# Optimization experiments

Hardware: AMD Instinct MI355X
Metric: run time of the kernel (lower is better)

The kernel has to match this reference:

```python
import jax, jax.numpy as jnp
import numpy as np
from jax import lax

K = 3        # kernel_size
PAD = 1      # padding
DIL = 1      # dilation
C_IN = 64
C_OUT = 64
B, H, W = 8, 128, 128


def conv2d(x, w, b, pad):
    # x: [n,c,h,w], w: [o,i,kh,kw], pad: (ph, pw)
    out = lax.conv_general_dilated(
        x, w, window_strides=(1, 1),
        padding=[(pad[0], pad[0]), (pad[1], pad[1])],
        rhs_dilation=(DIL, DIL),
        dimension_numbers=("NCHW", "OIHW", "NCHW"))
    return out + b[None, :, None, None]


def bilinear_sample(x, py, px):
    # x: [n,c,h,w]; py/px: [n,K,h,w] fractional sample coords (zeros outside).
    n, c, h, w = x.shape
    y0 = jnp.floor(py)
    x0 = jnp.floor(px)
    wy = py - y0  # frac weights
    wx = px - x0
    xf = x.reshape(n, c, h * w)

    def gather(yi, xi):
        valid = ((yi >= 0) & (yi < h) & (xi >= 0) & (xi < w)).astype(x.dtype)
        yc = jnp.clip(yi, 0, h - 1).astype(jnp.int32)
        xc = jnp.clip(xi, 0, w - 1).astype(jnp.int32)
        idx = (yc * w + xc).reshape(n, -1)  # [n, K*h*w]
        g = jax.vmap(lambda xb, ib: jnp.take(xb, ib, axis=1))(xf, idx)
        return g.reshape(n, c, *yi.shape[1:]), valid

    v00, m00 = gather(y0, x0)
    v01, m01 = gather(y0, x0 + 1)
    v10, m10 = gather(y0 + 1, x0)
    v11, m11 = gather(y0 + 1, x0 + 1)
    w00 = ((1 - wy) * (1 - wx) * m00)[:, None]
    w01 = ((1 - wy) * wx * m01)[:, None]
    w10 = (wy * (1 - wx) * m10)[:, None]
    w11 = (wy * wx * m11)[:, None]
    return v00 * w00 + v01 * w01 + v10 * w10 + v11 * w11  # [n,c,K,h,w]


def deform_conv_axial(x, offset, mask, w, b, ky_base, kx_base):
    # offset: [n,K,2,h,w] (dy, dx per tap); mask: [n,K,h,w]
    # ky_base/kx_base: [K] static tap displacements
    n, c, h, wd = x.shape
    ii = jnp.arange(h, dtype=x.dtype)[None, None, :, None]
    jj = jnp.arange(wd, dtype=x.dtype)[None, None, None, :]
    py = ii + ky_base[None, :, None, None] + offset[:, :, 0]
    px = jj + kx_base[None, :, None, None] + offset[:, :, 1]
    val = bilinear_sample(x, py, px) * mask[:, None]  # [n,c,K,h,w]
    out = jnp.einsum('nckhw,ock->nohw', val, w.reshape(w.shape[0], c, K))
    return out + b[None, :, None, None]


def setup_inputs() -> dict:
    key = jax.random.key(0)
    ks = jax.random.split(key, 14)
    sc = 0.05
    d = {
        'x': jax.random.normal(ks[0], (B, C_IN, H, W), dtype=jnp.float32),
        'w_off_h': jax.random.normal(ks[1], (2 * K, C_IN, 1, K), dtype=jnp.float32) * sc,
        'b_off_h': jnp.zeros((2 * K,), dtype=jnp.float32),
        'w_mask_h': jax.random.normal(ks[2], (K, C_IN, 1, K), dtype=jnp.float32) * sc,
        'b_mask_h': jnp.zeros((K,), dtype=jnp.float32),
        'w_off_v': jax.random.normal(ks[3], (2 * K, C_IN, K, 1), dtype=jnp.float32) * sc,
        'b_off_v': jnp.zeros((2 * K,), dtype=jnp.float32),
        'w_mask_v': jax.random.normal(ks[4], (K, C_IN, K, 1), dtype=jnp.float32) * sc,
        'b_mask_v': jnp.zeros((K,), dtype=jnp.float32),
        'w_h': jax.random.normal(ks[5], (C_OUT, C_IN, 1, K), dtype=jnp.float32) * (1.0 / np.sqrt(C_IN * K)),
        'b_h': jax.random.normal(ks[6], (C_OUT,), dtype=jnp.float32) * 0.01,
        'w_v': jax.random.normal(ks[7], (C_OUT, C_OUT, K, 1), dtype=jnp.float32) * (1.0 / np.sqrt(C_OUT * K)),
        'b_v': jax.random.normal(ks[8], (C_OUT,), dtype=jnp.float32) * 0.01,
    }
    return d


def reference(x, w_off_h, b_off_h, w_mask_h, b_mask_h, w_off_v, b_off_v,
              w_mask_v, b_mask_v, w_h, b_h, w_v, b_v):
    n, c, h, w = x.shape
    taps = jnp.arange(K, dtype=x.dtype) * DIL - PAD  # [-1,0,1] for K=3,pad=1
    zeros_k = jnp.zeros((K,), dtype=x.dtype)

    # Horizontal pass: offsets/masks from x, deformable (1,K) conv on x
    offset_h = conv2d(x, w_off_h, b_off_h, (0, PAD)).reshape(n, K, 2, h, w)
    mask_h = jax.nn.sigmoid(conv2d(x, w_mask_h, b_mask_h, (0, PAD)))  # [n,K,h,w]
    x_h = deform_conv_axial(x, offset_h, mask_h, w_h, b_h, zeros_k, taps)

    # Vertical pass: offsets/masks from x, deformable (K,1) conv on x_h
    offset_v = conv2d(x, w_off_v, b_off_v, (PAD, 0)).reshape(n, K, 2, h, w)
    mask_v = jax.nn.sigmoid(conv2d(x, w_mask_v, b_mask_v, (PAD, 0)))
    x_v = deform_conv_axial(x_h, offset_v, mask_v, w_v, b_v, taps, zeros_k)
    return x_v
```

## Files before the change

kernel.cpp:

```cpp
#include <hip/hip_runtime.h>

#define C_ 64
#define H_ 128
#define W_ 128
#define B_ 8
#define HW_ (H_*W_)
#define NPIX (B_*HW_)

typedef _Float16 half8 __attribute__((ext_vector_type(8)));
typedef _Float16 half4 __attribute__((ext_vector_type(4)));
typedef float floatx4 __attribute__((ext_vector_type(4)));

#define RDL_I(v, l) __builtin_amdgcn_readlane((v), (l))
#define RDL_F(v, l) __builtin_bit_cast(float, \
    __builtin_amdgcn_readlane(__builtin_bit_cast(int, (v)), (l)))

__global__ __launch_bounds__(256, 8) void setup_kernel(
    const float* __restrict__ x, _Float16* __restrict__ xT,
    const float* __restrict__ w_off_h, const float* __restrict__ w_mask_h,
    const float* __restrict__ w_off_v, const float* __restrict__ w_mask_v,
    const float* __restrict__ w_h, const float* __restrict__ w_v,
    float* __restrict__ wOffAll, _Float16* __restrict__ wF16_h,
    _Float16* __restrict__ wF16_v)
{
    int gid = blockIdx.x * 256 + threadIdx.x;
    if (gid < 64 * 56) {
        int c = gid / 56, idx = gid - 56 * c;
        float v = 0.f;
        if (idx < 18)      v = w_off_h [((idx      ) / 3) * 192 + c * 3 + (idx      ) % 3];
        else if (idx < 27) v = w_mask_h[((idx - 18) / 3) * 192 + c * 3 + (idx - 18) % 3];
        else if (idx < 45) v = w_off_v [((idx - 27) / 3) * 192 + c * 3 + (idx - 27) % 3];
        else if (idx < 54) v = w_mask_v[((idx - 45) / 3) * 192 + c * 3 + (idx - 45) % 3];
        wOffAll[c * 56 + idx] = v;
    } else if (gid < 3584 + 24576) {
        int i = gid - 3584;
        if (i < 12288) {
            int o = i / 192, rem = i - o * 192;
            int c = rem / 3, k = rem - 3 * c;
            wF16_h[o * 192 + k * 64 + c] = (_Float16)w_h[i];
        } else {
            i -= 12288;
            int o = i / 192, rem = i - o * 192;
            int c = rem / 3, k = rem - 3 * c;
            wF16_v[o * 192 + k * 64 + c] = (_Float16)w_v[i];
        }
    }

    __shared__ _Float16 tile[64][66];
    int lane = threadIdx.x & 63;
    int wv   = threadIdx.x >> 6;
    int bid = blockIdx.x;
    int n = bid & 7;
    int m = bid >> 3;
    const float* xs = x + (size_t)n * C_ * HW_ + (size_t)m * 64;
    #pragma unroll
    for (int cc = 0; cc < 16; ++cc) {
        int c = wv * 16 + cc;
        tile[c][lane] = (_Float16)xs[(size_t)c * HW_ + lane];
    }
    __syncthreads();
    _Float16* xd = xT + ((size_t)n * HW_ + (size_t)m * 64) * 64;
    #pragma unroll
    for (int pp = 0; pp < 16; ++pp) {
        int p = wv * 16 + pp;
        xd[(size_t)p * 64 + lane] = tile[lane][p];
    }
}

#define SWIZZLE_NP()                        \
    int bid = blockIdx.x;                   \
    int n   = bid & 7;                      \
    int m   = bid >> 3;       \
    int pix = m * 64 + lane;                \
    int j = pix & (W_ - 1);                 \
    int i = pix >> 7;

#define TAP_WAVE48(DYE, DXE, MME, KYO, KXO)                                   \
    int   tI  = 0;                                                            \
    float tw0 = 0.f, tw1 = 0.f, tw2 = 0.f, tw3 = 0.f;                         \
    {                                                                         \
        int li = lane / 3, k = lane - 3 * li;                                 \
        if (lane < 48) {                                                      \
            int p = (li < 8) ? (wv * 8 + li) : (32 + wv * 8 + (li - 8));      \
            int pixp = m * 64 + p;                                            \
            float dy = (DYE);                                                 \
            float dx = (DXE);                                                 \
            float mm = (MME);                                                 \
            float fi = (float)(pixp >> 7), fj = (float)(pixp & (W_ - 1));     \
            float py = fi + (float)(KYO) + dy;                                \
            float px = fj + (float)(KXO) + dx;                                \
            float y0f = floorf(py), x0f = floorf(px);                         \
            float wy = py - y0f, wx = px - x0f;                               \
            int y0 = (int)y0f, x0 = (int)x0f;                                 \
            int y1 = y0 + 1, x1 = x0 + 1;                                     \
            bool vy0 = (y0 >= 0) && (y0 < H_);                                \
            bool vy1 = (y1 >= 0) && (y1 < H_);                                \
            bool vx0 = (x0 >= 0) && (x0 < W_);                                \
            bool vx1 = (x1 >= 0) && (x1 < W_);                                \
            float wy1 = 1.f - wy, wx1 = 1.f - wx;                             \
            float w00 = (vy0 && vx0) ? wy1 * wx1 * mm : 0.f;                  \
            float w01 = (vy0 && vx1) ? wy1 * wx  * mm : 0.f;                  \
            float w10 = (vy1 && vx0) ? wy  * wx1 * mm : 0.f;                  \
            float w11 = (vy1 && vx1) ? wy  * wx  * mm : 0.f;                  \
            int y0c = min(max(y0, 0), H_ - 1), y1c = min(max(y1, 0), H_ - 1); \
            int x0c = min(max(x0, 0), W_ - 1), x1c = min(max(x1, 0), W_ - 1); \
            int yb = min(max(y0, 0), H_ - 2),  xb = min(max(x0, 0), W_ - 2);  \
            int r0 = y0c - yb, r1 = y1c - yb;                   \
            int cA = x0c - xb, cB = x1c - xb;                   \
            tw0 = ((r0==0)&&(cA==0)?w00:0.f) + ((r0==0)&&(cB==0)?w01:0.f)     \
                + ((r1==0)&&(cA==0)?w10:0.f) + ((r1==0)&&(cB==0)?w11:0.f);    \
            tw1 = ((r0==0)&&(cA==1)?w00:0.f) + ((r0==0)&&(cB==1)?w01:0.f)     \
                + ((r1==0)&&(cA==1)?w10:0.f) + ((r1==0)&&(cB==1)?w11:0.f);    \
            tw2 = ((r0==1)&&(cA==0)?w00:0.f) + ((r0==1)&&(cB==0)?w01:0.f)     \
                + ((r1==1)&&(cA==0)?w10:0.f) + ((r1==1)&&(cB==0)?w11:0.f);    \
            tw3 = ((r0==1)&&(cA==1)?w00:0.f) + ((r0==1)&&(cB==1)?w01:0.f)     \
                + ((r1==1)&&(cA==1)?w10:0.f) + ((r1==1)&&(cB==1)?w11:0.f);    \
            tI = (yb * W_ + xb) * 64;                                         \
        }                                                                     \
    }

#define GATHER_MFMA_BODY(ST)                                                  \
    int col = lane & 15;                                                      \
    floatx4 accT[4];                                                          \
    _Pragma("unroll")                                                         \
    for (int T = 0; T < 4; ++T) accT[T] = floatx4{0.f, 0.f, 0.f, 0.f};        \
    _Pragma("unroll")                                                         \
    for (int hf = 0; hf < 2; ++hf) {                                          \
        _Pragma("unroll")                                                     \
        for (int q = 0; q < 8; ++q) {                                         \
            int r = wv * 8 + q;                                               \
            _Pragma("unroll")                                                 \
            for (int k = 0; k < 3; ++k) {                                     \
                const int tl = (hf * 8 + q) * 3 + k;                          \
                int ex   = RDL_I(tI, tl);                                     \
                float w0 = RDL_F(tw0, tl);                                    \
                float w1 = RDL_F(tw1, tl);                                    \
                float w2 = RDL_F(tw2, tl);                                    \
                float w3 = RDL_F(tw3, tl);                                    \
                const _Float16* cb = (ST) + ex;                               \
                float v00 = (float)cb[lane];                                  \
                float v01 = (float)cb[lane + 64];                             \
                float v10 = (float)cb[lane + 64 * W_];                        \
                float v11 = (float)cb[lane + 64 * W_ + 64];                   \
                float v = fmaf(w0, v00, fmaf(w1, v01,                         \
                          fmaf(w2, v10, w3 * v11)));                          \
                valT[r][k * 64 + lane] = (_Float16)v;                         \
            }                                                                 \
        }                                                                     \
        __syncthreads();                                                      \
        const _Float16* wpA = wF16 + (size_t)(c0 + (lane & 15)) * 192         \
                            + ((lane >> 4) << 3);                             \
        half8 A0 = *((const half8*)(wpA +   0));                              \
        half8 A1 = *((const half8*)(wpA +  32));                              \
        half8 A2 = *((const half8*)(wpA +  64));                              \
        half8 A3 = *((const half8*)(wpA +  96));                              \
        half8 A4 = *((const half8*)(wpA + 128));                              \
        half8 A5 = *((const half8*)(wpA + 160));                              \
        _Pragma("unroll")                                                     \
        for (int tt = 0; tt < 2; ++tt) {                                      \
            int T = hf * 2 + tt;                                              \
            const _Float16* bp = &valT[tt * 16 + col][(lane >> 4) << 3];      \
            floatx4 acc = accT[T];                                            \
            acc = __builtin_amdgcn_mfma_f32_16x16x32_f16(A0, *((const half8*)(bp +   0)), acc, 0, 0, 0); \
            acc = __builtin_amdgcn_mfma_f32_16x16x32_f16(A1, *((const half8*)(bp +  32)), acc, 0, 0, 0); \
            acc = __builtin_amdgcn_mfma_f32_16x16x32_f16(A2, *((const half8*)(bp +  64)), acc, 0, 0, 0); \
            acc = __builtin_amdgcn_mfma_f32_16x16x32_f16(A3, *((const half8*)(bp +  96)), acc, 0, 0, 0); \
            acc = __builtin_amdgcn_mfma_f32_16x16x32_f16(A4, *((const half8*)(bp + 128)), acc, 0, 0, 0); \
            acc = __builtin_amdgcn_mfma_f32_16x16x32_f16(A5, *((const half8*)(bp + 160)), acc, 0, 0, 0); \
            accT[T] = acc;                                                    \
        }                                                                     \
        if (hf == 0) __syncthreads();                                         \
    }

__global__ __launch_bounds__(256, 8) void deform_h_kernel(
    const float* __restrict__ x, const _Float16* __restrict__ xT,
    const float* __restrict__ wOffAll,
    const float* __restrict__ b_off_h, const float* __restrict__ b_mask_h,
    const float* __restrict__ b_off_v, const float* __restrict__ b_mask_v,
    const _Float16* __restrict__ wF16, const float* __restrict__ bias,
    float* __restrict__ off_v, float* __restrict__ mask_v,
    _Float16* __restrict__ x_hT)
{
    __shared__ __align__(16) char smem[18432];
    float (*red)[18][64] = reinterpret_cast<float(*)[18][64]>(smem);
    float (*red0)[64]    = reinterpret_cast<float(*)[64]>(smem);
    _Float16 (*valT)[200] = reinterpret_cast<_Float16(*)[200]>(smem);

    int lane = threadIdx.x & 63;
    int wv   = threadIdx.x >> 6;
    int c0 = __builtin_amdgcn_readfirstlane(wv << 4);

    SWIZZLE_NP();

    float a[18];
    #pragma unroll
    for (int o = 0; o < 18; ++o) a[o] = 0.f;

    const float* xs = x + (size_t)n * C_ * HW_ + (size_t)c0 * HW_;
    for (int cc = 0; cc < 16; ++cc) {
        const float* s = xs + cc * HW_;
        float xc = s[pix];
        float xl = (j > 0)      ? s[pix - 1]  : 0.f;
        float xr = (j < W_ - 1) ? s[pix + 1]  : 0.f;
        float xu = (i > 0)      ? s[pix - W_] : 0.f;
        float xd = (i < H_ - 1) ? s[pix + W_] : 0.f;
        const float* wc = wOffAll + (c0 + cc) * 56;
        #pragma unroll
        for (int o = 0; o < 6; ++o) {
            a[o]   = fmaf(xl, wc[3*o],    fmaf(xc, wc[3*o+1],    fmaf(xr, wc[3*o+2],    a[o])));
            a[9+o] = fmaf(xu, wc[27+3*o], fmaf(xc, wc[27+3*o+1], fmaf(xd, wc[27+3*o+2], a[9+o])));
        }
        #pragma unroll
        for (int o = 0; o < 3; ++o) {
            a[6+o]  = fmaf(xl, wc[18+3*o], fmaf(xc, wc[18+3*o+1], fmaf(xr, wc[18+3*o+2], a[6+o])));
            a[15+o] = fmaf(xu, wc[45+3*o], fmaf(xc, wc[45+3*o+1], fmaf(xd, wc[45+3*o+2], a[15+o])));
        }
    }

    #pragma unroll
    for (int o = 0; o < 18; ++o) red[wv][o][lane] = a[o];
    __syncthreads();

    for (int v = threadIdx.x; v < 18 * 64; v += 256) {
        int idx = v >> 6;
        int px  = v & 63;
        float sum = red[0][idx][px] + red[1][idx][px]
                  + red[2][idx][px] + red[3][idx][px];
        int pixg = m * 64 + px;
        if (idx < 6) {
            red[0][idx][px] = sum + b_off_h[idx];
        } else if (idx < 9) {
            red[0][idx][px] = 1.f / (1.f + __expf(-(sum + b_mask_h[idx - 6])));
        } else if (idx < 15) {
            off_v[((size_t)n * 6 + (idx - 9)) * HW_ + pixg] = sum + b_off_v[idx - 9];
        } else {
            mask_v[((size_t)n * 3 + (idx - 15)) * HW_ + pixg] =
                1.f / (1.f + __expf(-(sum + b_mask_v[idx - 15])));
        }
    }
    __syncthreads();

    TAP_WAVE48(red0[2*k][p], red0[2*k + 1][p], red0[6 + k][p], 0, (k - 1))
    __syncthreads();

    const _Float16* sT = xT + (size_t)n * (HW_ * 64);
    GATHER_MFMA_BODY(sT)

    int orow = c0 + ((lane >> 4) << 2);
    floatx4 bv = *((const floatx4*)&bias[orow]);
    _Float16* hb = x_hT + ((size_t)n * HW_ + (size_t)m * 64) * 64 + orow;
    #pragma unroll
    for (int T = 0; T < 4; ++T) {
        half4 o;
        o[0] = (_Float16)(accT[T][0] + bv[0]);
        o[1] = (_Float16)(accT[T][1] + bv[1]);
        o[2] = (_Float16)(accT[T][2] + bv[2]);
        o[3] = (_Float16)(accT[T][3] + bv[3]);
        *((half4*)(hb + (size_t)(T * 16 + col) * 64)) = o;
    }
}

__global__ __launch_bounds__(256, 8) void deform_v_kernel(
    const _Float16* __restrict__ srcT, const float* __restrict__ off,
    const float* __restrict__ mask, const _Float16* __restrict__ wF16,
    const float* __restrict__ bias, float* __restrict__ out)
{
    __shared__ __align__(16) _Float16 valT[32][200];

    int lane = threadIdx.x & 63;
    int wv   = threadIdx.x >> 6;
    int c0 = __builtin_amdgcn_readfirstlane(wv << 4);

    int bid = blockIdx.x;
    int n   = bid & 7;
    int m   = bid >> 3;

    TAP_WAVE48(off[(((size_t)n * 3 + k) * 2 + 0) * HW_ + pixp],
               off[(((size_t)n * 3 + k) * 2 + 1) * HW_ + pixp],
               mask[((size_t)n * 3 + k) * HW_ + pixp], (k - 1), 0)

    const _Float16* sT = srcT + (size_t)n * (HW_ * 64);
    GATHER_MFMA_BODY(sT)

    int orow = c0 + ((lane >> 4) << 2);
    floatx4 bv = *((const floatx4*)&bias[orow]);
    float* ob = out + ((size_t)n * C_ + orow) * HW_ + m * 64 + col;
    #pragma unroll
    for (int T = 0; T < 4; ++T) {
        __builtin_nontemporal_store(accT[T][0] + bv[0], &ob[T * 16 + (size_t)0 * HW_]);
        __builtin_nontemporal_store(accT[T][1] + bv[1], &ob[T * 16 + (size_t)1 * HW_]);
        __builtin_nontemporal_store(accT[T][2] + bv[2], &ob[T * 16 + (size_t)2 * HW_]);
        __builtin_nontemporal_store(accT[T][3] + bv[3], &ob[T * 16 + (size_t)3 * HW_]);
    }
}

extern "C" void kernel_launch(void* const* d_in, const int* in_sizes, int n_in,
                              void* d_out, int out_size, void* d_ws, size_t ws_size,
                              hipStream_t stream)
{
    const float* x        = (const float*)d_in[0];
    const float* w_off_h  = (const float*)d_in[1];
    const float* b_off_h  = (const float*)d_in[2];
    const float* w_mask_h = (const float*)d_in[3];
    const float* b_mask_h = (const float*)d_in[4];
    const float* w_off_v  = (const float*)d_in[5];
    const float* b_off_v  = (const float*)d_in[6];
    const float* w_mask_v = (const float*)d_in[7];
    const float* b_mask_v = (const float*)d_in[8];
    const float* w_h      = (const float*)d_in[9];
    const float* b_h      = (const float*)d_in[10];
    const float* w_v      = (const float*)d_in[11];
    const float* b_v      = (const float*)d_in[12];

    float* ws      = (float*)d_ws;
    float* off_v   = ws;
    float* mask_v  = off_v  + 786432;
    float* wOffAll = mask_v + 393216;
    _Float16* xT     = (_Float16*)(wOffAll + 3584);
    _Float16* x_hT   = xT + 8388608;
    _Float16* wF16_h = x_hT + 8388608;
    _Float16* wF16_v = wF16_h + 12288;

    dim3 grid(NPIX / 64), block(256);

    setup_kernel<<<grid, block, 0, stream>>>(
        x, xT, w_off_h, w_mask_h, w_off_v, w_mask_v, w_h, w_v,
        wOffAll, wF16_h, wF16_v);

    deform_h_kernel<<<grid, block, 0, stream>>>(
        x, xT, wOffAll, b_off_h, b_mask_h, b_off_v, b_mask_v,
        wF16_h, b_h, off_v, mask_v, x_hT);

    deform_v_kernel<<<grid, block, 0, stream>>>(
        x_hT, off_v, mask_v, wF16_v, b_v, (float*)d_out);
}
```

Baseline: 188.5 us.

## Move offset/mask stencil into transpose kernel and slim the horizontal deform kernel

Splits the small weight-prep work into its own tiny launch. When the workspace is large enough, it fuses the x transpose with the offset/mask stencil convolutions in one kernel, which writes horizontal and vertical offsets and masks to global memory. A slimmed horizontal deform kernel then only gathers and runs the MFMA. This moves the heavy register-using stencil out of the gather/MFMA kernel, at the cost of an extra launch and extra global traffic for off_h/mask_h. A fallback path keeps the old fused deform_h structure, with the transpose as a separate kernel.

New measurement: 187.7 us. Within noise of the previous version (-0.4%).

```diff
diff --git a/kernel.cpp b/kernel.cpp
--- a/kernel.cpp
+++ b/kernel.cpp
@@ -15,8 +15,7 @@
 #define RDL_F(v, l) __builtin_bit_cast(float, \
     __builtin_amdgcn_readlane(__builtin_bit_cast(int, (v)), (l)))
 
-__global__ __launch_bounds__(256, 8) void setup_kernel(
-    const float* __restrict__ x, _Float16* __restrict__ xT,
+__global__ __launch_bounds__(256) void prep_kernel(
     const float* __restrict__ w_off_h, const float* __restrict__ w_mask_h,
     const float* __restrict__ w_off_v, const float* __restrict__ w_mask_v,
     const float* __restrict__ w_h, const float* __restrict__ w_v,
@@ -45,26 +44,6 @@
             wF16_v[o * 192 + k * 64 + c] = (_Float16)w_v[i];
         }
     }
-
-    __shared__ _Float16 tile[64][66];
-    int lane = threadIdx.x & 63;
-    int wv   = threadIdx.x >> 6;
-    int bid = blockIdx.x;
-    int n = bid & 7;
-    int m = bid >> 3;
-    const float* xs = x + (size_t)n * C_ * HW_ + (size_t)m * 64;
-    #pragma unroll
-    for (int cc = 0; cc < 16; ++cc) {
-        int c = wv * 16 + cc;
-        tile[c][lane] = (_Float16)xs[(size_t)c * HW_ + lane];
-    }
-    __syncthreads();
-    _Float16* xd = xT + ((size_t)n * HW_ + (size_t)m * 64) * 64;
-    #pragma unroll
-    for (int pp = 0; pp < 16; ++pp) {
-        int p = wv * 16 + pp;
-        xd[(size_t)p * 64 + lane] = tile[lane][p];
-    }
 }
 
 #define SWIZZLE_NP()                        \
@@ -74,6 +53,109 @@
     int pix = m * 64 + lane;                \
     int j = pix & (W_ - 1);                 \
     int i = pix >> 7;
+
+#define TRANSPOSE_PHASE(TILE)                                                 \
+    {                                                                         \
+        const float* xs_t = x + (size_t)n * C_ * HW_ + (size_t)m * 64;        \
+        _Pragma("unroll")                                                     \
+        for (int cc = 0; cc < 16; ++cc) {                                     \
+            int c = wv * 16 + cc;                                             \
+            (TILE)[c][lane] = (_Float16)xs_t[(size_t)c * HW_ + lane];         \
+        }                                                                     \
+        __syncthreads();                                                      \
+        _Float16* xd = xT + ((size_t)n * HW_ + (size_t)m * 64) * 64;          \
+        _Pragma("unroll")                                                     \
+        for (int pp = 0; pp < 16; ++pp) {                                     \
+            int p = wv * 16 + pp;                                             \
+            xd[(size_t)p * 64 + lane] = (TILE)[lane][p];                      \
+        }                                                                     \
+    }
+
+#define PROLOGUE_STENCIL()                                                    \
+    float a[18];                                                              \
+    _Pragma("unroll")                                                         \
+    for (int o = 0; o < 18; ++o) a[o] = 0.f;                                  \
+    {                                                                         \
+        const float* xs = x + (size_t)n * C_ * HW_ + (size_t)c0 * HW_;        \
+        for (int cc = 0; cc < 16; ++cc) {                                     \
+            const float* s = xs + cc * HW_;                                   \
+            float xc = s[pix];                                                \
+            float xl = (j > 0)      ? s[pix - 1]  : 0.f;                      \
+            float xr = (j < W_ - 1) ? s[pix + 1]  : 0.f;                      \
+            float xu = (i > 0)      ? s[pix - W_] : 0.f;                      \
+            float xd2 = (i < H_ - 1) ? s[pix + W_] : 0.f;                     \
+            const float* wc = wOffAll + (c0 + cc) * 56;                       \
+            _Pragma("unroll")                                                 \
+            for (int o = 0; o < 6; ++o) {                                     \
+                a[o]   = fmaf(xl, wc[3*o],    fmaf(xc, wc[3*o+1],    fmaf(xr, wc[3*o+2],    a[o])));    \
+                a[9+o] = fmaf(xu, wc[27+3*o], fmaf(xc, wc[27+3*o+1], fmaf(xd2, wc[27+3*o+2], a[9+o]))); \
+            }                                                                 \
+            _Pragma("unroll")                                                 \
+            for (int o = 0; o < 3; ++o) {                                     \
+                a[6+o]  = fmaf(xl, wc[18+3*o], fmaf(xc, wc[18+3*o+1], fmaf(xr, wc[18+3*o+2], a[6+o])));    \
+                a[15+o] = fmaf(xu, wc[45+3*o], fmaf(xc, wc[45+3*o+1], fmaf(xd2, wc[45+3*o+2], a[15+o]))); \
+            }                                                                 \
+        }                                                                     \
+    }
+
+__global__ __launch_bounds__(256, 8) void setup_big_kernel(
+    const float* __restrict__ x, _Float16* __restrict__ xT,
+    const float* __restrict__ wOffAll,
+    const float* __restrict__ b_off_h, const float* __restrict__ b_mask_h,
+    const float* __restrict__ b_off_v, const float* __restrict__ b_mask_v,
+    float* __restrict__ off_h, float* __restrict__ mask_h,
+    float* __restrict__ off_v, float* __restrict__ mask_v)
+{
+    __shared__ __align__(16) char smem[18432];
+    _Float16 (*tile)[66] = reinterpret_cast<_Float16(*)[66]>(smem);
+    float (*red)[18][64] = reinterpret_cast<float(*)[18][64]>(smem);
+
+    int lane = threadIdx.x & 63;
+    int wv   = threadIdx.x >> 6;
+    int c0 = __builtin_amdgcn_readfirstlane(wv << 4);
+
+    SWIZZLE_NP();
+
+    TRANSPOSE_PHASE(tile)
+    __syncthreads();
+
+    PROLOGUE_STENCIL()
+
+    #pragma unroll
+    for (int o = 0; o < 18; ++o) red[wv][o][lane] = a[o];
+    __syncthreads();
+
+    for (int v = threadIdx.x; v < 18 * 64; v += 256) {
+        int idx = v >> 6;
+        int px  = v & 63;
+        float sum = red[0][idx][px] + red[1][idx][px]
+                  + red[2][idx][px] + red[3][idx][px];
+        int pixg = m * 64 + px;
+        if (idx < 6) {
+            off_h[((size_t)n * 6 + idx) * HW_ + pixg] = sum + b_off_h[idx];
+        } else if (idx < 9) {
+            mask_h[((size_t)n * 3 + (idx - 6)) * HW_ + pixg] =
+                1.f / (1.f + __expf(-(sum + b_mask_h[idx - 6])));
+        } else if (idx < 15) {
+            off_v[((size_t)n * 6 + (idx - 9)) * HW_ + pixg] = sum + b_off_v[idx - 9];
+        } else {
+            mask_v[((size_t)n * 3 + (idx - 15)) * HW_ + pixg] =
+                1.f / (1.f + __expf(-(sum + b_mask_v[idx - 15])));
+        }
+    }
+}
+
+__global__ __launch_bounds__(256, 8) void transpose_kernel(
+    const float* __restrict__ x, _Float16* __restrict__ xT)
+{
+    __shared__ _Float16 tile[64][66];
+    int lane = threadIdx.x & 63;
+    int wv   = threadIdx.x >> 6;
+    int bid = blockIdx.x;
+    int n = bid & 7;
+    int m = bid >> 3;
+    TRANSPOSE_PHASE(tile)
+}
 
 #define TAP_WAVE48(DYE, DXE, MME, KYO, KXO)                                   \
     int   tI  = 0;                                                            \
@@ -172,7 +254,43 @@
         if (hf == 0) __syncthreads();                                         \
     }
 
-__global__ __launch_bounds__(256, 8) void deform_h_kernel(
+__global__ __launch_bounds__(256, 8) void deform_h_slim_kernel(
+    const _Float16* __restrict__ srcT, const float* __restrict__ off,
+    const float* __restrict__ mask, const _Float16* __restrict__ wF16,
+    const float* __restrict__ bias, _Float16* __restrict__ x_hT)
+{
+    __shared__ __align__(16) _Float16 valT[32][200];
+
+    int lane = threadIdx.x & 63;
+    int wv   = threadIdx.x >> 6;
+    int c0 = __builtin_amdgcn_readfirstlane(wv << 4);
+
+    int bid = blockIdx.x;
+    int n   = bid & 7;
+    int m   = bid >> 3;
+
+    TAP_WAVE48(off[(((size_t)n * 3 + k) * 2 + 0) * HW_ + pixp],
+               off[(((size_t)n * 3 + k) * 2 + 1) * HW_ + pixp],
+               mask[((size_t)n * 3 + k) * HW_ + pixp], 0, (k - 1))
+
+    const _Float16* sT = srcT + (size_t)n * (HW_ * 64);
+    GATHER_MFMA_BODY(sT)
+
+    int orow = c0 + ((lane >> 4) << 2);
+    floatx4 bv = *((const floatx4*)&bias[orow]);
+    _Float16* hb = x_hT + ((size_t)n * HW_ + (size_t)m * 64) * 64 + orow;
+    #pragma unroll
+    for (int T = 0; T < 4; ++T) {
+        half4 o;
+        o[0] = (_Float16)(accT[T][0] + bv[0]);
+        o[1] = (_Float16)(accT[T][1] + bv[1]);
+        o[2] = (_Float16)(accT[T][2] + bv[2]);
+        o[3] = (_Float16)(accT[T][3] + bv[3]);
+        *((half4*)(hb + (size_t)(T * 16 + col) * 64)) = o;
+    }
+}
+
+__global__ __launch_bounds__(256, 8) void deform_h_full_kernel(
     const float* __restrict__ x, const _Float16* __restrict__ xT,
     const float* __restrict__ wOffAll,
     const float* __restrict__ b_off_h, const float* __restrict__ b_mask_h,
@@ -192,30 +310,7 @@
 
     SWIZZLE_NP();
 
-    float a[18];
-    #pragma unroll
-    for (int o = 0; o < 18; ++o) a[o] = 0.f;
-
-    const float* xs = x + (size_t)n * C_ * HW_ + (size_t)c0 * HW_;
-    for (int cc = 0; cc < 16; ++cc) {
-        const float* s = xs + cc * HW_;
-        float xc = s[pix];
-        float xl = (j > 0)      ? s[pix - 1]  : 0.f;
-        float xr = (j < W_ - 1) ? s[pix + 1]  : 0.f;
-        float xu = (i > 0)      ? s[pix - W_] : 0.f;
-        float xd = (i < H_ - 1) ? s[pix + W_] : 0.f;
-        const float* wc = wOffAll + (c0 + cc) * 56;
-        #pragma unroll
-        for (int o = 0; o < 6; ++o) {
-            a[o]   = fmaf(xl, wc[3*o],    fmaf(xc, wc[3*o+1],    fmaf(xr, wc[3*o+2],    a[o])));
-            a[9+o] = fmaf(xu, wc[27+3*o], fmaf(xc, wc[27+3*o+1], fmaf(xd, wc[27+3*o+2], a[9+o])));
-        }
-        #pragma unroll
-        for (int o = 0; o < 3; ++o) {
-            a[6+o]  = fmaf(xl, wc[18+3*o], fmaf(xc, wc[18+3*o+1], fmaf(xr, wc[18+3*o+2], a[6+o])));
-            a[15+o] = fmaf(xu, wc[45+3*o], fmaf(xc, wc[45+3*o+1], fmaf(xd, wc[45+3*o+2], a[15+o])));
-        }
-    }
+    PROLOGUE_STENCIL()
 
     #pragma unroll
     for (int o = 0; o < 18; ++o) red[wv][o][lane] = a[o];
@@ -315,22 +410,52 @@
     float* ws      = (float*)d_ws;
     float* off_v   = ws;
     float* mask_v  = off_v  + 786432;
-    float* wOffAll = mask_v + 393216;
-    _Float16* xT     = (_Float16*)(wOffAll + 3584);
-    _Float16* x_hT   = xT + 8388608;
-    _Float16* wF16_h = x_hT + 8388608;
-    _Float16* wF16_v = wF16_h + 12288;
 
     dim3 grid(NPIX / 64), block(256);
 
-    setup_kernel<<<grid, block, 0, stream>>>(
-        x, xT, w_off_h, w_mask_h, w_off_v, w_mask_v, w_h, w_v,
-        wOffAll, wF16_h, wF16_v);
-
-    deform_h_kernel<<<grid, block, 0, stream>>>(
-        x, xT, wOffAll, b_off_h, b_mask_h, b_off_v, b_mask_v,
-        wF16_h, b_h, off_v, mask_v, x_hT);
-
-    deform_v_kernel<<<grid, block, 0, stream>>>(
-        x_hT, off_v, mask_v, wF16_v, b_v, (float*)d_out);
-}
+    size_t need_big = (size_t)(786432 + 393216) * 2 * 4 + 3584 * 4
+                    + (size_t)(8388608 * 2 + 12288 * 2) * 2;
+
+    if (ws_size >= need_big) {
+        float* off_h   = mask_v + 393216;
+        float* mask_h  = off_h  + 786432;
+        float* wOffAll = mask_h + 393216;
+        _Float16* xT     = (_Float16*)(wOffAll + 3584);
+        _Float16* x_hT   = xT + 8388608;
+        _Float16* wF16_h = x_hT + 8388608;
+        _Float16* wF16_v = wF16_h + 12288;
+
+        prep_kernel<<<110, 256, 0, stream>>>(
+            w_off_h, w_mask_h, w_off_v, w_mask_v, w_h, w_v,
+            wOffAll, wF16_h, wF16_v);
+
+        setup_big_kernel<<<grid, block, 0, stream>>>(
+            x, xT, wOffAll, b_off_h, b_mask_h, b_off_v, b_mask_v,
+            off_h, mask_h, off_v, mask_v);
+
+        deform_h_slim_kernel<<<grid, block, 0, stream>>>(
+            xT, off_h, mask_h, wF16_h, b_h, x_hT);
+
+        deform_v_kernel<<<grid, block, 0, stream>>>(
+            x_hT, off_v, mask_v, wF16_v, b_v, (float*)d_out);
+    } else {
+        float* wOffAll = mask_v + 393216;
+        _Float16* xT     = (_Float16*)(wOffAll + 3584);
+        _Float16* x_hT   = xT + 8388608;
+        _Float16* wF16_h = x_hT + 8388608;
+        _Float16* wF16_v = wF16_h + 12288;
+
+        prep_kernel<<<110, 256, 0, stream>>>(
+            w_off_h, w_mask_h, w_off_v, w_mask_v, w_h, w_v,
+            wOffAll, wF16_h, wF16_v);
+
+        transpose_kernel<<<grid, block, 0, stream>>>(x, xT);
+
+        deform_h_full_kernel<<<grid, block, 0, stream>>>(
+            x, xT, wOffAll, b_off_h, b_mask_h, b_off_v, b_mask_v,
+            wF16_h, b_h, off_v, mask_v, x_hT);
+
+        deform_v_kernel<<<grid, block, 0, stream>>>(
+            x_hT, off_v, mask_v, wF16_v, b_v, (float*)d_out);
+    }
+}
```
